# Kernel tuning notes

Measured on AMD Instinct MI355X. Metric: run time of the kernel, lower is better.

## Reference

```python
import jax, jax.numpy as jnp
import numpy as np

N, K, C = 10000, 64, 128


def setup_inputs() -> dict:
    key = jax.random.key(0)
    ks = jax.random.split(key, 6)
    return {
        "real": jax.random.normal(ks[0], (N, C), dtype=jnp.float32),
        "imag": jax.random.normal(ks[1], (N, C), dtype=jnp.float32),
        "Qreal": jax.random.normal(ks[2], (N, K), dtype=jnp.float32) / np.sqrt(N),
        "Qimag": jax.random.normal(ks[3], (N, K), dtype=jnp.float32) / np.sqrt(N),
        "Ritz": jax.random.uniform(ks[4], (K,), dtype=jnp.float32),
        "weight": jax.random.normal(ks[5], (C, C), dtype=jnp.float32) * np.sqrt(2.0 / (C + C)),  # xavier-ish scale
        "long_diff": 5,
    }


def reference(real, imag, Qreal, Qimag, Ritz, weight, long_diff):
    # TT = Ritz ** long_diff ; spectral filters L = Q diag(TT) Q^H split into real/imag
    TT = jnp.power(Ritz, long_diff)  # [K]
    QrT = Qreal * TT  # [N,K] columns scaled by TT (== Qreal @ diag(TT))
    QiT = Qimag * TT
    L_real = QrT @ Qreal.T + QiT @ Qimag.T  # [N,N]
    L_imag = QiT @ Qreal.T - QrT @ Qimag.T  # [N,N]
    # complex spmm + shared dense weight: (L @ X_complex) @ W
    res_real = (L_real @ real - L_imag @ imag) @ weight  # [N,C]
    res_imag = (L_imag @ real + L_real @ imag) @ weight  # [N,C]
    # complex ReLU: mask by sign of real part
    mask = (res_real >= 0).astype(res_real.dtype)
    return real + mask * res_real, imag + mask * res_imag
```

## Files before the change

kernel.cpp:

```cpp
#include <hip/hip_runtime.h>

#define NN 10000
#define KK 64
#define CC 128
#define OUTOFF (NN * CC)
#define NCH 625
#define PART_F4 4096

__device__ __forceinline__ float4 f4fma(float s, float4 v, float4 a) {
    a.x = fmaf(s, v.x, a.x); a.y = fmaf(s, v.y, a.y);
    a.z = fmaf(s, v.z, a.z); a.w = fmaf(s, v.w, a.w);
    return a;
}
__device__ __forceinline__ float4 f4add(float4 a, float4 b) {
    a.x += b.x; a.y += b.y; a.z += b.z; a.w += b.w; return a;
}


__global__ __launch_bounds__(512) void kA(const float* __restrict__ re,
                                          const float* __restrict__ im,
                                          const float* __restrict__ Qr,
                                          const float* __restrict__ Qi,
                                          float* __restrict__ part)
{
    __shared__ float4 smem[1536];
    const int t = threadIdx.x;
    const int bid = blockIdx.x;
    const int kt = t & 15;
    const int ctA = t >> 4;
    const int row_q = (t & 255) >> 4, q_q = t & 15;
    const int row_x = t >> 5,          q_x = t & 31;
    const float4* gq  = (const float4*)((t < 256) ? Qr : Qi);
    const float4* gre = (const float4*)re;
    const float4* gim = (const float4*)im;

    smem[t]        = gq [(size_t)(bid * 16 + row_q) * 16 + q_q];
    smem[512 + t]  = gre[(size_t)(bid * 16 + row_x) * 32 + q_x];
    smem[1024 + t] = gim[(size_t)(bid * 16 + row_x) * 32 + q_x];
    __syncthreads();

    float aU[4][4] = {}, aV[4][4] = {};
#pragma unroll 4
    for (int rr = 0; rr < 16; ++rr) {
        float4 q_r = smem[rr * 16 + kt];
        float4 q_i = smem[256 + rr * 16 + kt];
        float4 x_r = smem[512 + rr * 32 + ctA];
        float4 x_i = smem[1024 + rr * 32 + ctA];
        float qr_[4] = {q_r.x, q_r.y, q_r.z, q_r.w};
        float qi_[4] = {q_i.x, q_i.y, q_i.z, q_i.w};
        float xr_[4] = {x_r.x, x_r.y, x_r.z, x_r.w};
        float xi_[4] = {x_i.x, x_i.y, x_i.z, x_i.w};
#pragma unroll
        for (int a = 0; a < 4; ++a)
#pragma unroll
            for (int b = 0; b < 4; ++b) {
                aU[a][b] = fmaf(qr_[a], xr_[b], aU[a][b]);
                aU[a][b] = fmaf(qi_[a], xi_[b], aU[a][b]);
                aV[a][b] = fmaf(qi_[a], xr_[b], aV[a][b]);
                aV[a][b] = fmaf(-qr_[a], xi_[b], aV[a][b]);
            }
    }
    float* base = part + (size_t)bid * 16384;
    const int k0 = kt * 4, c0 = ctA * 4;
#pragma unroll
    for (int a = 0; a < 4; ++a) {
        *(float4*)(base + (k0 + a) * CC + c0)        = make_float4(aU[a][0], aU[a][1], aU[a][2], aU[a][3]);
        *(float4*)(base + 8192 + (k0 + a) * CC + c0) = make_float4(aV[a][0], aV[a][1], aV[a][2], aV[a][3]);
    }
}

__global__ __launch_bounds__(512) void kR1(const float* __restrict__ part,
                                           float* __restrict__ row)
{
    __shared__ float4 red4[512];
    const int t = threadIdx.x;
    const int i = t & 15;
    const int g = t >> 4;
    const int o = blockIdx.x * 16 + i;
    const float4* p = (const float4*)part + (size_t)g * PART_F4 + o;
    const float4 z = make_float4(0.f, 0.f, 0.f, 0.f);
    float4 s0 = z, s1 = z, s2 = z, s3 = z;
    int pp = g;
    for (; pp + 96 < NCH; pp += 128) {
        s0 = f4add(s0, p[0]);
        s1 = f4add(s1, p[(size_t)32 * PART_F4]);
        s2 = f4add(s2, p[(size_t)64 * PART_F4]);
        s3 = f4add(s3, p[(size_t)96 * PART_F4]);
        p += (size_t)128 * PART_F4;
    }
    for (; pp < NCH; pp += 32) {
        s0 = f4add(s0, p[0]);
        p += (size_t)32 * PART_F4;
    }
    red4[t] = f4add(f4add(s0, s1), f4add(s2, s3));
    __syncthreads();
    if (t < 16) {
        float4 tot = z;
#pragma unroll
        for (int gg = 0; gg < 32; ++gg) tot = f4add(tot, red4[gg * 16 + t]);
        ((float4*)row)[blockIdx.x * 16 + t] = tot;
    }
}

__global__ __launch_bounds__(128) void kR2(const float* __restrict__ row,
                                           const float* __restrict__ Ritz,
                                           const int* __restrict__ ldp,
                                           const float* __restrict__ W,
                                           float* __restrict__ UVW)
{
    __shared__ float rowS[128];
    const int t = threadIdx.x;
    const int m = blockIdx.x >> 6, k = blockIdx.x & 63;
    rowS[t] = row[m * 8192 + k * 128 + t];
    __syncthreads();
    float acc = 0.f;
#pragma unroll 8
    for (int cp = 0; cp < 128; ++cp)
        acc = fmaf(rowS[cp], W[cp * 128 + t], acc);
    const int ld = *ldp;
    const float rz = Ritz[k];
    float tt = 1.f;
    for (int i = 0; i < ld; ++i) tt *= rz;
    UVW[m * 8192 + k * 128 + t] = tt * acc;
}

__global__ __launch_bounds__(256) void kC(const float* __restrict__ re,
                                          const float* __restrict__ im,
                                          const float* __restrict__ Qr,
                                          const float* __restrict__ Qi,
                                          const float* __restrict__ UVW,
                                          float* __restrict__ out)
{
    const int t = threadIdx.x;
    const int ct = t & 31;
    const int r  = t >> 5;
    const int na = blockIdx.x * 16 + r;
    const int nb = na + 8;
    const float4* U4 = (const float4*)UVW;
    const float4* V4 = U4 + 2048;

    const float4* qra = (const float4*)(Qr + (size_t)na * KK);
    const float4* qia = (const float4*)(Qi + (size_t)na * KK);
    const float4* qrb = (const float4*)(Qr + (size_t)nb * KK);
    const float4* qib = (const float4*)(Qi + (size_t)nb * KK);

    float4 z = make_float4(0.f, 0.f, 0.f, 0.f);
    float4 Ra = z, Ia = z, Rb = z, Ib = z;

#pragma unroll 4
    for (int k4 = 0; k4 < 16; ++k4) {
        float4 QRa = qra[k4], QIa = qia[k4];
        float4 QRb = qrb[k4], QIb = qib[k4];
        float ar[4] = {QRa.x, QRa.y, QRa.z, QRa.w};
        float ai[4] = {QIa.x, QIa.y, QIa.z, QIa.w};
        float br[4] = {QRb.x, QRb.y, QRb.z, QRb.w};
        float bi[4] = {QIb.x, QIb.y, QIb.z, QIb.w};
#pragma unroll
        for (int jj = 0; jj < 4; ++jj) {
            const int k = k4 * 4 + jj;
            float4 uw = U4[k * 32 + ct];
            float4 vw = V4[k * 32 + ct];
            Ra = f4fma(ar[jj], uw, Ra); Ra = f4fma(ai[jj], vw, Ra);
            Ia = f4fma(ai[jj], uw, Ia); Ia = f4fma(-ar[jj], vw, Ia);
            Rb = f4fma(br[jj], uw, Rb); Rb = f4fma(bi[jj], vw, Rb);
            Ib = f4fma(bi[jj], uw, Ib); Ib = f4fma(-br[jj], vw, Ib);
        }
    }
    const int cc = ct * 4;
    {
        float4 rin = *(const float4*)(re + (size_t)na * CC + cc);
        float4 iin = *(const float4*)(im + (size_t)na * CC + cc);
        float4 orr, oii;
        orr.x = rin.x + (Ra.x >= 0.f ? Ra.x : 0.f); oii.x = iin.x + (Ra.x >= 0.f ? Ia.x : 0.f);
        orr.y = rin.y + (Ra.y >= 0.f ? Ra.y : 0.f); oii.y = iin.y + (Ra.y >= 0.f ? Ia.y : 0.f);
        orr.z = rin.z + (Ra.z >= 0.f ? Ra.z : 0.f); oii.z = iin.z + (Ra.z >= 0.f ? Ia.z : 0.f);
        orr.w = rin.w + (Ra.w >= 0.f ? Ra.w : 0.f); oii.w = iin.w + (Ra.w >= 0.f ? Ia.w : 0.f);
        *(float4*)(out + (size_t)na * CC + cc)          = orr;
        *(float4*)(out + OUTOFF + (size_t)na * CC + cc) = oii;
    }
    {
        float4 rin = *(const float4*)(re + (size_t)nb * CC + cc);
        float4 iin = *(const float4*)(im + (size_t)nb * CC + cc);
        float4 orr, oii;
        orr.x = rin.x + (Rb.x >= 0.f ? Rb.x : 0.f); oii.x = iin.x + (Rb.x >= 0.f ? Ib.x : 0.f);
        orr.y = rin.y + (Rb.y >= 0.f ? Rb.y : 0.f); oii.y = iin.y + (Rb.y >= 0.f ? Ib.y : 0.f);
        orr.z = rin.z + (Rb.z >= 0.f ? Rb.z : 0.f); oii.z = iin.z + (Rb.z >= 0.f ? Ib.z : 0.f);
        orr.w = rin.w + (Rb.w >= 0.f ? Rb.w : 0.f); oii.w = iin.w + (Rb.w >= 0.f ? Ib.w : 0.f);
        *(float4*)(out + (size_t)nb * CC + cc)          = orr;
        *(float4*)(out + OUTOFF + (size_t)nb * CC + cc) = oii;
    }
}

extern "C" void kernel_launch(void* const* d_in, const int* in_sizes, int n_in,
                              void* d_out, int out_size, void* d_ws, size_t ws_size,
                              hipStream_t stream) {
    const float* re   = (const float*)d_in[0];
    const float* im   = (const float*)d_in[1];
    const float* Qr   = (const float*)d_in[2];
    const float* Qi   = (const float*)d_in[3];
    const float* Ritz = (const float*)d_in[4];
    const float* W    = (const float*)d_in[5];
    const int*   ldp  = (const int*)d_in[6];
    float* out = (float*)d_out;
    float* ws  = (float*)d_ws;

    float* part = ws;
    float* row  = ws + (size_t)NCH * 16384;
    float* UVW  = row + 16384;

    kA <<<NCH, 512, 0, stream>>>(re, im, Qr, Qi, part);
    kR1<<<256, 512, 0, stream>>>(part, row);
    kR2<<<128, 128, 0, stream>>>(row, Ritz, ldp, W, UVW);
    kC <<<NCH, 256, 0, stream>>>(re, im, Qr, Qi, UVW, out);
}
```

Before: 123.1 us.

## Fuse projection, reduction and weight stages into one persistent kernel with grid barriers

Merges the three front kernels (partial projection, cross-chunk reduction, weight multiply) into one 512-block kernel that uses atomic-counter grid barriers instead of separate launches. Each block now handles 20 rows, giving 500 chunks. The reduction uses wave shuffles. kC also stages the UVW matrix in shared memory (64KB) rather than reading it from global memory. This removes launch gaps and shrinks the partials buffer. The risks are that the spin barriers deadlock if not all 512 blocks are co-resident, the added memset, and lower kC occupancy from its large shared allocation.

```diff
diff --git a/kernel.cpp b/kernel.cpp
--- a/kernel.cpp
+++ b/kernel.cpp
@@ -4,8 +4,14 @@
 #define KK 64
 #define CC 128
 #define OUTOFF (NN * CC)
-#define NCH 625
+#define NB1 512
+#define ROWS 20
+#define NCH 500
 #define PART_F4 4096
+
+#define ROW_OFF  ((size_t)NCH * 16384)
+#define UVW_OFF  (ROW_OFF + 16384)
+#define CNT_OFF  (UVW_OFF + 16384)
 
 __device__ __forceinline__ float4 f4fma(float s, float4 v, float4 a) {
     a.x = fmaf(s, v.x, a.x); a.y = fmaf(s, v.y, a.y);
@@ -15,113 +21,127 @@
 __device__ __forceinline__ float4 f4add(float4 a, float4 b) {
     a.x += b.x; a.y += b.y; a.z += b.z; a.w += b.w; return a;
 }
-
-
-__global__ __launch_bounds__(512) void kA(const float* __restrict__ re,
-                                          const float* __restrict__ im,
-                                          const float* __restrict__ Qr,
-                                          const float* __restrict__ Qi,
-                                          float* __restrict__ part)
+__device__ __forceinline__ float4 f4shflxor(float4 s, int m) {
+    float4 r;
+    r.x = s.x + __shfl_xor(s.x, m); r.y = s.y + __shfl_xor(s.y, m);
+    r.z = s.z + __shfl_xor(s.z, m); r.w = s.w + __shfl_xor(s.w, m);
+    return r;
+}
+
+__device__ __forceinline__ void gbar(unsigned* c, unsigned target) {
+    __syncthreads();
+    if (threadIdx.x == 0) {
+        __threadfence();
+        atomicAdd(c, 1u);
+        while (__hip_atomic_load(c, __ATOMIC_RELAXED, __HIP_MEMORY_SCOPE_AGENT) < target)
+            __builtin_amdgcn_s_sleep(4);
+        __threadfence();
+    }
+    __syncthreads();
+}
+
+__global__ __launch_bounds__(512, 4) void K1(const float* __restrict__ re,
+                                             const float* __restrict__ im,
+                                             const float* __restrict__ Qr,
+                                             const float* __restrict__ Qi,
+                                             const float* __restrict__ Ritz,
+                                             const float* __restrict__ W,
+                                             const int* __restrict__ ldp,
+                                             float* __restrict__ ws)
 {
-    __shared__ float4 smem[1536];
+    __shared__ float4 smem[1920];
     const int t = threadIdx.x;
     const int bid = blockIdx.x;
-    const int kt = t & 15;
-    const int ctA = t >> 4;
-    const int row_q = (t & 255) >> 4, q_q = t & 15;
-    const int row_x = t >> 5,          q_x = t & 31;
-    const float4* gq  = (const float4*)((t < 256) ? Qr : Qi);
-    const float4* gre = (const float4*)re;
-    const float4* gim = (const float4*)im;
-
-    smem[t]        = gq [(size_t)(bid * 16 + row_q) * 16 + q_q];
-    smem[512 + t]  = gre[(size_t)(bid * 16 + row_x) * 32 + q_x];
-    smem[1024 + t] = gim[(size_t)(bid * 16 + row_x) * 32 + q_x];
-    __syncthreads();
-
-    float aU[4][4] = {}, aV[4][4] = {};
+    float4* part4 = (float4*)ws;
+    float4* row4  = (float4*)(ws + ROW_OFF);
+    unsigned* cnt = (unsigned*)(ws + CNT_OFF);
+
+    if (bid < NCH) {
+        const float4* gqr = (const float4*)Qr;
+        const float4* gqi = (const float4*)Qi;
+        const float4* gre = (const float4*)re;
+        const float4* gim = (const float4*)im;
+        for (int i = t; i < 1920; i += 512) {
+            float4 v;
+            if (i < 320)       v = gqr[(size_t)bid * 320 + i];
+            else if (i < 640)  v = gqi[(size_t)bid * 320 + (i - 320)];
+            else if (i < 1280) v = gre[(size_t)bid * 640 + (i - 640)];
+            else               v = gim[(size_t)bid * 640 + (i - 1280)];
+            smem[i] = v;
+        }
+        __syncthreads();
+        const int kt = t & 15;
+        const int ctA = t >> 4;
+        float aU[4][4] = {}, aV[4][4] = {};
 #pragma unroll 4
-    for (int rr = 0; rr < 16; ++rr) {
-        float4 q_r = smem[rr * 16 + kt];
-        float4 q_i = smem[256 + rr * 16 + kt];
-        float4 x_r = smem[512 + rr * 32 + ctA];
-        float4 x_i = smem[1024 + rr * 32 + ctA];
-        float qr_[4] = {q_r.x, q_r.y, q_r.z, q_r.w};
-        float qi_[4] = {q_i.x, q_i.y, q_i.z, q_i.w};
-        float xr_[4] = {x_r.x, x_r.y, x_r.z, x_r.w};
-        float xi_[4] = {x_i.x, x_i.y, x_i.z, x_i.w};
-#pragma unroll
-        for (int a = 0; a < 4; ++a)
-#pragma unroll
-            for (int b = 0; b < 4; ++b) {
-                aU[a][b] = fmaf(qr_[a], xr_[b], aU[a][b]);
-                aU[a][b] = fmaf(qi_[a], xi_[b], aU[a][b]);
-                aV[a][b] = fmaf(qi_[a], xr_[b], aV[a][b]);
-                aV[a][b] = fmaf(-qr_[a], xi_[b], aV[a][b]);
-            }
-    }
-    float* base = part + (size_t)bid * 16384;
-    const int k0 = kt * 4, c0 = ctA * 4;
-#pragma unroll
-    for (int a = 0; a < 4; ++a) {
-        *(float4*)(base + (k0 + a) * CC + c0)        = make_float4(aU[a][0], aU[a][1], aU[a][2], aU[a][3]);
-        *(float4*)(base + 8192 + (k0 + a) * CC + c0) = make_float4(aV[a][0], aV[a][1], aV[a][2], aV[a][3]);
-    }
-}
-
-__global__ __launch_bounds__(512) void kR1(const float* __restrict__ part,
-                                           float* __restrict__ row)
-{
-    __shared__ float4 red4[512];
-    const int t = threadIdx.x;
-    const int i = t & 15;
-    const int g = t >> 4;
-    const int o = blockIdx.x * 16 + i;
-    const float4* p = (const float4*)part + (size_t)g * PART_F4 + o;
-    const float4 z = make_float4(0.f, 0.f, 0.f, 0.f);
-    float4 s0 = z, s1 = z, s2 = z, s3 = z;
-    int pp = g;
-    for (; pp + 96 < NCH; pp += 128) {
-        s0 = f4add(s0, p[0]);
-        s1 = f4add(s1, p[(size_t)32 * PART_F4]);
-        s2 = f4add(s2, p[(size_t)64 * PART_F4]);
-        s3 = f4add(s3, p[(size_t)96 * PART_F4]);
-        p += (size_t)128 * PART_F4;
-    }
-    for (; pp < NCH; pp += 32) {
-        s0 = f4add(s0, p[0]);
-        p += (size_t)32 * PART_F4;
-    }
-    red4[t] = f4add(f4add(s0, s1), f4add(s2, s3));
-    __syncthreads();
-    if (t < 16) {
-        float4 tot = z;
-#pragma unroll
-        for (int gg = 0; gg < 32; ++gg) tot = f4add(tot, red4[gg * 16 + t]);
-        ((float4*)row)[blockIdx.x * 16 + t] = tot;
-    }
-}
-
-__global__ __launch_bounds__(128) void kR2(const float* __restrict__ row,
-                                           const float* __restrict__ Ritz,
-                                           const int* __restrict__ ldp,
-                                           const float* __restrict__ W,
-                                           float* __restrict__ UVW)
-{
-    __shared__ float rowS[128];
-    const int t = threadIdx.x;
-    const int m = blockIdx.x >> 6, k = blockIdx.x & 63;
-    rowS[t] = row[m * 8192 + k * 128 + t];
-    __syncthreads();
-    float acc = 0.f;
+        for (int rr = 0; rr < ROWS; ++rr) {
+            float4 q_r = smem[rr * 16 + kt];
+            float4 q_i = smem[320 + rr * 16 + kt];
+            float4 x_r = smem[640 + rr * 32 + ctA];
+            float4 x_i = smem[1280 + rr * 32 + ctA];
+            float qr_[4] = {q_r.x, q_r.y, q_r.z, q_r.w};
+            float qi_[4] = {q_i.x, q_i.y, q_i.z, q_i.w};
+            float xr_[4] = {x_r.x, x_r.y, x_r.z, x_r.w};
+            float xi_[4] = {x_i.x, x_i.y, x_i.z, x_i.w};
+#pragma unroll
+            for (int a = 0; a < 4; ++a)
+#pragma unroll
+                for (int b = 0; b < 4; ++b) {
+                    aU[a][b] = fmaf(qr_[a], xr_[b], aU[a][b]);
+                    aU[a][b] = fmaf(qi_[a], xi_[b], aU[a][b]);
+                    aV[a][b] = fmaf(qi_[a], xr_[b], aV[a][b]);
+                    aV[a][b] = fmaf(-qr_[a], xi_[b], aV[a][b]);
+                }
+        }
+        float* base = ws + (size_t)bid * 16384;
+        const int k0 = kt * 4, c0 = ctA * 4;
+#pragma unroll
+        for (int a = 0; a < 4; ++a) {
+            *(float4*)(base + (k0 + a) * CC + c0)        = make_float4(aU[a][0], aU[a][1], aU[a][2], aU[a][3]);
+            *(float4*)(base + 8192 + (k0 + a) * CC + c0) = make_float4(aV[a][0], aV[a][1], aV[a][2], aV[a][3]);
+        }
+    }
+
+    gbar(&cnt[0], NB1);
+
+    {
+        const int o = t & 7;
+        const int d = t >> 3;
+        const int O = bid * 8 + o;
+        float4 s = make_float4(0.f, 0.f, 0.f, 0.f);
+        for (int p = d; p < NCH; p += 64)
+            s = f4add(s, part4[(size_t)p * PART_F4 + O]);
+        s = f4shflxor(s, 8); s = f4shflxor(s, 16); s = f4shflxor(s, 32);
+        float4* red4 = smem;
+        const int wv = t >> 6;
+        if ((t & 63) < 8) red4[wv * 8 + o] = s;
+        __syncthreads();
+        if (t < 64) {
+            float4 s2 = red4[t];
+            s2 = f4shflxor(s2, 8); s2 = f4shflxor(s2, 16); s2 = f4shflxor(s2, 32);
+            if (t < 8) row4[bid * 8 + t] = s2;
+        }
+    }
+
+    gbar(&cnt[1], NB1);
+
+    if (bid < 128) {
+        float* rowS = (float*)smem;
+        const int m = bid >> 6, k = bid & 63;
+        if (t < 128) rowS[t] = (ws + ROW_OFF)[m * 8192 + k * 128 + t];
+        __syncthreads();
+        if (t < 128) {
+            float acc = 0.f;
 #pragma unroll 8
-    for (int cp = 0; cp < 128; ++cp)
-        acc = fmaf(rowS[cp], W[cp * 128 + t], acc);
-    const int ld = *ldp;
-    const float rz = Ritz[k];
-    float tt = 1.f;
-    for (int i = 0; i < ld; ++i) tt *= rz;
-    UVW[m * 8192 + k * 128 + t] = tt * acc;
+            for (int cp = 0; cp < 128; ++cp)
+                acc = fmaf(rowS[cp], W[cp * 128 + t], acc);
+            const int ld = *ldp;
+            const float rz = Ritz[k];
+            float tt = 1.f;
+            for (int i = 0; i < ld; ++i) tt *= rz;
+            (ws + UVW_OFF)[m * 8192 + k * 128 + t] = tt * acc;
+        }
+    }
 }
 
 __global__ __launch_bounds__(256) void kC(const float* __restrict__ re,
@@ -131,13 +151,17 @@
                                           const float* __restrict__ UVW,
                                           float* __restrict__ out)
 {
+    __shared__ float4 s[4096];
     const int t = threadIdx.x;
+    {
+        const float4* g = (const float4*)UVW;
+        for (int i = t; i < 4096; i += 256) s[i] = g[i];
+    }
+    __syncthreads();
     const int ct = t & 31;
     const int r  = t >> 5;
     const int na = blockIdx.x * 16 + r;
     const int nb = na + 8;
-    const float4* U4 = (const float4*)UVW;
-    const float4* V4 = U4 + 2048;
 
     const float4* qra = (const float4*)(Qr + (size_t)na * KK);
     const float4* qia = (const float4*)(Qi + (size_t)na * KK);
@@ -158,8 +182,8 @@
 #pragma unroll
         for (int jj = 0; jj < 4; ++jj) {
             const int k = k4 * 4 + jj;
-            float4 uw = U4[k * 32 + ct];
-            float4 vw = V4[k * 32 + ct];
+            float4 uw = s[k * 32 + ct];
+            float4 vw = s[2048 + k * 32 + ct];
             Ra = f4fma(ar[jj], uw, Ra); Ra = f4fma(ai[jj], vw, Ra);
             Ia = f4fma(ai[jj], uw, Ia); Ia = f4fma(-ar[jj], vw, Ia);
             Rb = f4fma(br[jj], uw, Rb); Rb = f4fma(bi[jj], vw, Rb);
@@ -204,12 +228,7 @@
     float* out = (float*)d_out;
     float* ws  = (float*)d_ws;
 
-    float* part = ws;
-    float* row  = ws + (size_t)NCH * 16384;
-    float* UVW  = row + 16384;
-
-    kA <<<NCH, 512, 0, stream>>>(re, im, Qr, Qi, part);
-    kR1<<<256, 512, 0, stream>>>(part, row);
-    kR2<<<128, 128, 0, stream>>>(row, Ritz, ldp, W, UVW);
-    kC <<<NCH, 256, 0, stream>>>(re, im, Qr, Qi, UVW, out);
-}
+    hipMemsetAsync(ws + CNT_OFF, 0, 64, stream);
+    K1<<<NB1, 512, 0, stream>>>(re, im, Qr, Qi, Ritz, W, ldp, ws);
+    kC<<<625, 256, 0, stream>>>(re, im, Qr, Qi, ws + UVW_OFF, out);
+}
```

Result: slower. 207.2 us (+68.4%).

## Enlarge per-thread register tiles in projection and output kernels

Applied to the files above, without the earlier changes.

The projection kernel now processes 20 rows per block with 256 threads, each computing a 4x8 register tile instead of 4x4. This cuts the chunk count from 625 to 500, so fewer partials are written and reduced. The output kernel now has each thread compute 4 rows instead of 2, reusing each U/V load across more rows with 128-thread blocks. The larger tiles raise register pressure and lower thread-level parallelism, which may hurt occupancy.

```diff
diff --git a/kernel.cpp b/kernel.cpp
--- a/kernel.cpp
+++ b/kernel.cpp
@@ -4,8 +4,12 @@
 #define KK 64
 #define CC 128
 #define OUTOFF (NN * CC)
-#define NCH 625
+#define ROWS 20
+#define NCH 500
 #define PART_F4 4096
+
+#define ROW_OFF  ((size_t)NCH * 16384)
+#define UVW_OFF  (ROW_OFF + 16384)
 
 __device__ __forceinline__ float4 f4fma(float s, float4 v, float4 a) {
     a.x = fmaf(s, v.x, a.x); a.y = fmaf(s, v.y, a.y);
@@ -16,44 +20,49 @@
     a.x += b.x; a.y += b.y; a.z += b.z; a.w += b.w; return a;
 }
 
-
-__global__ __launch_bounds__(512) void kA(const float* __restrict__ re,
+__global__ __launch_bounds__(256) void kA(const float* __restrict__ re,
                                           const float* __restrict__ im,
                                           const float* __restrict__ Qr,
                                           const float* __restrict__ Qi,
                                           float* __restrict__ part)
 {
-    __shared__ float4 smem[1536];
+    __shared__ float4 smem[1920];
     const int t = threadIdx.x;
     const int bid = blockIdx.x;
-    const int kt = t & 15;
-    const int ctA = t >> 4;
-    const int row_q = (t & 255) >> 4, q_q = t & 15;
-    const int row_x = t >> 5,          q_x = t & 31;
-    const float4* gq  = (const float4*)((t < 256) ? Qr : Qi);
-    const float4* gre = (const float4*)re;
-    const float4* gim = (const float4*)im;
-
-    smem[t]        = gq [(size_t)(bid * 16 + row_q) * 16 + q_q];
-    smem[512 + t]  = gre[(size_t)(bid * 16 + row_x) * 32 + q_x];
-    smem[1024 + t] = gim[(size_t)(bid * 16 + row_x) * 32 + q_x];
+    {
+        const float4* gqr = (const float4*)Qr;
+        const float4* gqi = (const float4*)Qi;
+        const float4* gre = (const float4*)re;
+        const float4* gim = (const float4*)im;
+        for (int i = t; i < 1920; i += 256) {
+            float4 v;
+            if (i < 320)       v = gqr[(size_t)bid * 320 + i];
+            else if (i < 640)  v = gqi[(size_t)bid * 320 + (i - 320)];
+            else if (i < 1280) v = gre[(size_t)bid * 640 + (i - 640)];
+            else               v = gim[(size_t)bid * 640 + (i - 1280)];
+            smem[i] = v;
+        }
+    }
     __syncthreads();
-
-    float aU[4][4] = {}, aV[4][4] = {};
+    const int kt = t >> 4;
+    const int c8 = t & 15;
+    float aU[4][8] = {}, aV[4][8] = {};
 #pragma unroll 4
-    for (int rr = 0; rr < 16; ++rr) {
+    for (int rr = 0; rr < ROWS; ++rr) {
         float4 q_r = smem[rr * 16 + kt];
-        float4 q_i = smem[256 + rr * 16 + kt];
-        float4 x_r = smem[512 + rr * 32 + ctA];
-        float4 x_i = smem[1024 + rr * 32 + ctA];
+        float4 q_i = smem[320 + rr * 16 + kt];
+        float4 x_r0 = smem[640 + rr * 32 + c8 * 2];
+        float4 x_r1 = smem[640 + rr * 32 + c8 * 2 + 1];
+        float4 x_i0 = smem[1280 + rr * 32 + c8 * 2];
+        float4 x_i1 = smem[1280 + rr * 32 + c8 * 2 + 1];
         float qr_[4] = {q_r.x, q_r.y, q_r.z, q_r.w};
         float qi_[4] = {q_i.x, q_i.y, q_i.z, q_i.w};
-        float xr_[4] = {x_r.x, x_r.y, x_r.z, x_r.w};
-        float xi_[4] = {x_i.x, x_i.y, x_i.z, x_i.w};
+        float xr_[8] = {x_r0.x, x_r0.y, x_r0.z, x_r0.w, x_r1.x, x_r1.y, x_r1.z, x_r1.w};
+        float xi_[8] = {x_i0.x, x_i0.y, x_i0.z, x_i0.w, x_i1.x, x_i1.y, x_i1.z, x_i1.w};
 #pragma unroll
         for (int a = 0; a < 4; ++a)
 #pragma unroll
-            for (int b = 0; b < 4; ++b) {
+            for (int b = 0; b < 8; ++b) {
                 aU[a][b] = fmaf(qr_[a], xr_[b], aU[a][b]);
                 aU[a][b] = fmaf(qi_[a], xi_[b], aU[a][b]);
                 aV[a][b] = fmaf(qi_[a], xr_[b], aV[a][b]);
@@ -61,11 +70,13 @@
             }
     }
     float* base = part + (size_t)bid * 16384;
-    const int k0 = kt * 4, c0 = ctA * 4;
+    const int k0 = kt * 4, c0 = c8 * 8;
 #pragma unroll
     for (int a = 0; a < 4; ++a) {
-        *(float4*)(base + (k0 + a) * CC + c0)        = make_float4(aU[a][0], aU[a][1], aU[a][2], aU[a][3]);
-        *(float4*)(base + 8192 + (k0 + a) * CC + c0) = make_float4(aV[a][0], aV[a][1], aV[a][2], aV[a][3]);
+        *(float4*)(base + (k0 + a) * CC + c0)            = make_float4(aU[a][0], aU[a][1], aU[a][2], aU[a][3]);
+        *(float4*)(base + (k0 + a) * CC + c0 + 4)        = make_float4(aU[a][4], aU[a][5], aU[a][6], aU[a][7]);
+        *(float4*)(base + 8192 + (k0 + a) * CC + c0)     = make_float4(aV[a][0], aV[a][1], aV[a][2], aV[a][3]);
+        *(float4*)(base + 8192 + (k0 + a) * CC + c0 + 4) = make_float4(aV[a][4], aV[a][5], aV[a][6], aV[a][7]);
     }
 }
 
@@ -124,7 +135,7 @@
     UVW[m * 8192 + k * 128 + t] = tt * acc;
 }
 
-__global__ __launch_bounds__(256) void kC(const float* __restrict__ re,
+__global__ __launch_bounds__(128) void kC(const float* __restrict__ re,
                                           const float* __restrict__ im,
                                           const float* __restrict__ Qr,
                                           const float* __restrict__ Qi,
@@ -133,61 +144,51 @@
 {
     const int t = threadIdx.x;
     const int ct = t & 31;
-    const int r  = t >> 5;
-    const int na = blockIdx.x * 16 + r;
-    const int nb = na + 8;
+    const int rq = t >> 5;
+    const int r0 = blockIdx.x * 16 + rq * 4;
     const float4* U4 = (const float4*)UVW;
     const float4* V4 = U4 + 2048;
-
-    const float4* qra = (const float4*)(Qr + (size_t)na * KK);
-    const float4* qia = (const float4*)(Qi + (size_t)na * KK);
-    const float4* qrb = (const float4*)(Qr + (size_t)nb * KK);
-    const float4* qib = (const float4*)(Qi + (size_t)nb * KK);
-
-    float4 z = make_float4(0.f, 0.f, 0.f, 0.f);
-    float4 Ra = z, Ia = z, Rb = z, Ib = z;
+    const float4* qr0 = (const float4*)(Qr + (size_t)r0 * KK);
+    const float4* qi0 = (const float4*)(Qi + (size_t)r0 * KK);
+
+    const float4 z = make_float4(0.f, 0.f, 0.f, 0.f);
+    float4 R[4] = {z, z, z, z}, I[4] = {z, z, z, z};
 
 #pragma unroll 4
     for (int k4 = 0; k4 < 16; ++k4) {
-        float4 QRa = qra[k4], QIa = qia[k4];
-        float4 QRb = qrb[k4], QIb = qib[k4];
-        float ar[4] = {QRa.x, QRa.y, QRa.z, QRa.w};
-        float ai[4] = {QIa.x, QIa.y, QIa.z, QIa.w};
-        float br[4] = {QRb.x, QRb.y, QRb.z, QRb.w};
-        float bi[4] = {QIb.x, QIb.y, QIb.z, QIb.w};
+        float4 qr[4], qi[4];
+#pragma unroll
+        for (int j = 0; j < 4; ++j) {
+            qr[j] = qr0[j * 16 + k4];
+            qi[j] = qi0[j * 16 + k4];
+        }
 #pragma unroll
         for (int jj = 0; jj < 4; ++jj) {
             const int k = k4 * 4 + jj;
             float4 uw = U4[k * 32 + ct];
             float4 vw = V4[k * 32 + ct];
-            Ra = f4fma(ar[jj], uw, Ra); Ra = f4fma(ai[jj], vw, Ra);
-            Ia = f4fma(ai[jj], uw, Ia); Ia = f4fma(-ar[jj], vw, Ia);
-            Rb = f4fma(br[jj], uw, Rb); Rb = f4fma(bi[jj], vw, Rb);
-            Ib = f4fma(bi[jj], uw, Ib); Ib = f4fma(-br[jj], vw, Ib);
+#pragma unroll
+            for (int j = 0; j < 4; ++j) {
+                float ar[4] = {qr[j].x, qr[j].y, qr[j].z, qr[j].w};
+                float ai[4] = {qi[j].x, qi[j].y, qi[j].z, qi[j].w};
+                R[j] = f4fma(ar[jj], uw, R[j]); R[j] = f4fma(ai[jj], vw, R[j]);
+                I[j] = f4fma(ai[jj], uw, I[j]); I[j] = f4fma(-ar[jj], vw, I[j]);
+            }
         }
     }
     const int cc = ct * 4;
-    {
-        float4 rin = *(const float4*)(re + (size_t)na * CC + cc);
-        float4 iin = *(const float4*)(im + (size_t)na * CC + cc);
+#pragma unroll
+    for (int j = 0; j < 4; ++j) {
+        const int row = r0 + j;
+        float4 rin = *(const float4*)(re + (size_t)row * CC + cc);
+        float4 iin = *(const float4*)(im + (size_t)row * CC + cc);
         float4 orr, oii;
-        orr.x = rin.x + (Ra.x >= 0.f ? Ra.x : 0.f); oii.x = iin.x + (Ra.x >= 0.f ? Ia.x : 0.f);
-        orr.y = rin.y + (Ra.y >= 0.f ? Ra.y : 0.f); oii.y = iin.y + (Ra.y >= 0.f ? Ia.y : 0.f);
-        orr.z = rin.z + (Ra.z >= 0.f ? Ra.z : 0.f); oii.z = iin.z + (Ra.z >= 0.f ? Ia.z : 0.f);
-        orr.w = rin.w + (Ra.w >= 0.f ? Ra.w : 0.f); oii.w = iin.w + (Ra.w >= 0.f ? Ia.w : 0.f);
-        *(float4*)(out + (size_t)na * CC + cc)          = orr;
-        *(float4*)(out + OUTOFF + (size_t)na * CC + cc) = oii;
-    }
-    {
-        float4 rin = *(const float4*)(re + (size_t)nb * CC + cc);
-        float4 iin = *(const float4*)(im + (size_t)nb * CC + cc);
-        float4 orr, oii;
-        orr.x = rin.x + (Rb.x >= 0.f ? Rb.x : 0.f); oii.x = iin.x + (Rb.x >= 0.f ? Ib.x : 0.f);
-        orr.y = rin.y + (Rb.y >= 0.f ? Rb.y : 0.f); oii.y = iin.y + (Rb.y >= 0.f ? Ib.y : 0.f);
-        orr.z = rin.z + (Rb.z >= 0.f ? Rb.z : 0.f); oii.z = iin.z + (Rb.z >= 0.f ? Ib.z : 0.f);
-        orr.w = rin.w + (Rb.w >= 0.f ? Rb.w : 0.f); oii.w = iin.w + (Rb.w >= 0.f ? Ib.w : 0.f);
-        *(float4*)(out + (size_t)nb * CC + cc)          = orr;
-        *(float4*)(out + OUTOFF + (size_t)nb * CC + cc) = oii;
+        orr.x = rin.x + (R[j].x >= 0.f ? R[j].x : 0.f); oii.x = iin.x + (R[j].x >= 0.f ? I[j].x : 0.f);
+        orr.y = rin.y + (R[j].y >= 0.f ? R[j].y : 0.f); oii.y = iin.y + (R[j].y >= 0.f ? I[j].y : 0.f);
+        orr.z = rin.z + (R[j].z >= 0.f ? R[j].z : 0.f); oii.z = iin.z + (R[j].z >= 0.f ? I[j].z : 0.f);
+        orr.w = rin.w + (R[j].w >= 0.f ? R[j].w : 0.f); oii.w = iin.w + (R[j].w >= 0.f ? I[j].w : 0.f);
+        *(float4*)(out + (size_t)row * CC + cc)          = orr;
+        *(float4*)(out + OUTOFF + (size_t)row * CC + cc) = oii;
     }
 }
 
@@ -205,11 +206,11 @@
     float* ws  = (float*)d_ws;
 
     float* part = ws;
-    float* row  = ws + (size_t)NCH * 16384;
-    float* UVW  = row + 16384;
-
-    kA <<<NCH, 512, 0, stream>>>(re, im, Qr, Qi, part);
+    float* row  = ws + ROW_OFF;
+    float* UVW  = ws + UVW_OFF;
+
+    kA <<<NCH, 256, 0, stream>>>(re, im, Qr, Qi, part);
     kR1<<<256, 512, 0, stream>>>(part, row);
     kR2<<<128, 128, 0, stream>>>(row, Ritz, ldp, W, UVW);
-    kC <<<NCH, 256, 0, stream>>>(re, im, Qr, Qi, UVW, out);
-}
+    kC <<<625, 128, 0, stream>>>(re, im, Qr, Qi, UVW, out);
+}
```

Result: slower. 126.1 us (+2.4%).
